# Kernel optimization log

Hardware: AMD Instinct MI355X
Metric: run time of the kernel (lower is better)

The kernel has to match this reference:

```python
import jax, jax.numpy as jnp
import numpy as np
from jax import lax

EOS_IDX = -1
N_POWERS = 7
B, L, D2 = 64, 81, 512      # batch, spatial_size, 2*inter_emb_size
S, C = 17, 256              # decode steps, candidates per step
V, H, E, P, F = 13042, 512, 80, 60, 178  # vocab, lstm_size, order_emb, power_emb, order-feat dim


def _lstm_cell(x, h, c, w_ih, w_hh, b_ih, b_hh):
    gates = x @ w_ih.T + b_ih + h @ w_hh.T + b_hh
    i, f, g, o = jnp.split(gates, 4, axis=-1)
    c_new = jax.nn.sigmoid(f) * c + jax.nn.sigmoid(i) * jnp.tanh(g)
    h_new = jax.nn.sigmoid(o) * jnp.tanh(c_new)
    return h_new, c_new


def _order_loc_feats(locs, enc_w, lin=None):
    # gather enc_w rows at candidate order locations; masked add == index_add_ with unique flat indices
    b = enc_w.shape[0]
    valid = locs > 0                                   # [B, C]
    safe = jnp.clip(locs, 0, enc_w.shape[1] - 1)
    g = enc_w[jnp.arange(b)[:, None], safe]            # [B, C, D]
    if lin is not None:
        g = g @ lin[0] + lin[1]
    return jnp.where(valid[..., None], g, jnp.zeros((), enc_w.dtype))


def setup_inputs() -> dict:
    key = jax.random.key(0)
    ks = jax.random.split(key, 40)
    w = lambda i, shape: jax.random.normal(ks[i], shape, dtype=jnp.float32) * 0.05
    return {
        'enc': jax.random.normal(ks[0], (B, L, D2), dtype=jnp.float32),
        'loc_idxs': jax.random.randint(ks[1], (B, L), 0, S),
        'all_cand_idxs': jax.random.randint(ks[2], (B, S, C), 0, V),
        'power': jax.random.randint(ks[3], (B, S), 0, N_POWERS),
        'teacher_force_orders': jax.random.randint(ks[4], (B, S), 0, V),
        'master_alignments': jax.random.uniform(ks[5], (L, L), dtype=jnp.float32),
        'order_embedding_w': w(6, (V, E)),
        'cand_embedding_w': w(7, (V, H)),
        'power_lin_w': w(8, (N_POWERS, P)),
        'power_lin_b': w(9, (P,)),
        'lstm_w_ih0': w(10, (4 * H, D2 + E + P)),
        'lstm_w_hh0': w(11, (4 * H, H)),
        'lstm_b_ih0': w(12, (4 * H,)),
        'lstm_b_hh0': w(13, (4 * H,)),
        'lstm_w_ih1': w(14, (4 * H, H)),
        'lstm_w_hh1': w(15, (4 * H, H)),
        'lstm_b_ih1': w(16, (4 * H,)),
        'lstm_b_hh1': w(17, (4 * H,)),
        'order_feats': jax.random.uniform(ks[18], (V, F), dtype=jnp.float32),
        'order_feat_lin_w': w(19, (F, E)),
        'order_feat_lin_b': w(20, (E,)),
        'order_decoder_w_w': w(21, (F, H)),
        'order_decoder_w_b': w(22, (H,)),
        'order_decoder_b_w': w(23, (F, 1)),
        'order_decoder_b_b': w(24, (1,)),
        'relfeat_src_w': w(25, (D2, H + 1)),
        'relfeat_src_b': w(26, (H + 1,)),
        'relfeat_dst_w': w(27, (D2, H + 1)),
        'relfeat_dst_b': w(28, (H + 1,)),
        'emb_relfeat_src_w': w(29, (E, H + 1)),
        'emb_relfeat_src_b': w(30, (H + 1,)),
        'emb_relfeat_dst_w': w(31, (E, H + 1)),
        'emb_relfeat_dst_b': w(32, (H + 1,)),
        'order_srcs': jax.random.randint(ks[33], (V,), -1, L),
        'order_dsts': jax.random.randint(ks[34], (V,), -1, L),
    }


def reference(enc, loc_idxs, all_cand_idxs, power, teacher_force_orders, master_alignments,
              order_embedding_w, cand_embedding_w, power_lin_w, power_lin_b,
              lstm_w_ih0, lstm_w_hh0, lstm_b_ih0, lstm_b_hh0,
              lstm_w_ih1, lstm_w_hh1, lstm_b_ih1, lstm_b_hh1,
              order_feats, order_feat_lin_w, order_feat_lin_b,
              order_decoder_w_w, order_decoder_w_b, order_decoder_b_w, order_decoder_b_b,
              relfeat_src_w, relfeat_src_b, relfeat_dst_w, relfeat_dst_b,
              emb_relfeat_src_w, emb_relfeat_src_b, emb_relfeat_dst_w, emb_relfeat_dst_b,
              order_srcs, order_dsts):
    b, l, d2 = enc.shape
    s = all_cand_idxs.shape[1]
    hsz = cand_embedding_w.shape[1]
    esz = order_embedding_w.shape[1]

    # compute_alignments for all steps at once: [S, B, L]
    steps = jnp.arange(s)
    mask = ((loc_idxs[None] == steps[:, None, None]) | (loc_idxs[None] == -2)).astype(enc.dtype)
    align = jnp.einsum('sbl,lm->sbm', mask, master_alignments)
    align = align / (align.sum(-1, keepdims=True) + 1e-5)
    loc_enc_all = jnp.einsum('sbl,bld->sbd', align, enc)            # [S, B, D2]

    power_1h = jax.nn.one_hot(jnp.clip(power, 0), N_POWERS, dtype=enc.dtype)
    power_embs = power_1h @ power_lin_w + power_lin_b               # [B, S, P]

    src_relfeat = enc @ relfeat_src_w + relfeat_src_b               # [B, L, H+1]
    dst_relfeat = enc @ relfeat_dst_w + relfeat_dst_b
    order_enc = jnp.zeros((b, l, esz), enc.dtype)                   # zeros per original init

    def body(carry, xs):
        h, c, order_emb = carry
        loc_enc, power_emb, cand_idxs, teacher = xs
        x = jnp.concatenate([loc_enc, order_emb, power_emb], axis=-1)
        h0, c0 = _lstm_cell(x, h[0], c[0], lstm_w_ih0, lstm_w_hh0, lstm_b_ih0, lstm_b_hh0)
        h1, c1 = _lstm_cell(h0, h[1], c[1], lstm_w_ih1, lstm_w_hh1, lstm_b_ih1, lstm_b_hh1)
        out = h1                                                    # [B, H]
        valid = cand_idxs != EOS_IDX
        safe_cand = jnp.clip(cand_idxs, 0)
        cand_emb = jnp.where(valid[..., None], cand_embedding_w[safe_cand], 0.0)
        logits = jnp.einsum('bch,bh->bc', cand_emb, out)
        feats = order_feats[safe_cand]                              # [B, C, F]
        order_w = jnp.concatenate([feats @ order_decoder_w_w + order_decoder_w_b,
                                   feats @ order_decoder_b_w + order_decoder_b_b], axis=-1)
        cand_srcs = order_srcs[safe_cand]
        cand_dsts = order_dsts[safe_cand]
        order_w = order_w + _order_loc_feats(cand_srcs, src_relfeat)
        order_w = order_w + _order_loc_feats(cand_dsts, dst_relfeat)
        order_w = order_w + _order_loc_feats(cand_srcs, order_enc, (emb_relfeat_src_w, emb_relfeat_src_b))
        order_w = order_w + _order_loc_feats(cand_dsts, order_enc, (emb_relfeat_dst_w, emb_relfeat_dst_b))
        out1 = jnp.concatenate([out, jnp.ones((out.shape[0], 1), out.dtype)], axis=-1)
        logits = logits + jnp.einsum('bcf,bf->bc', order_w, out1)
        logits = jnp.where(valid, logits, -1e9)
        local = jnp.argmax((cand_idxs == teacher[:, None]).astype(jnp.int32), axis=1)
        new_order_emb = order_embedding_w[teacher] + order_feats[teacher] @ order_feat_lin_w + order_feat_lin_b
        return (jnp.stack([h0, h1]), jnp.stack([c0, c1]), new_order_emb), (logits, local)

    init = (jnp.zeros((2, b, hsz), enc.dtype), jnp.zeros((2, b, hsz), enc.dtype), jnp.zeros((b, esz), enc.dtype))
    xs = (loc_enc_all, jnp.swapaxes(power_embs, 0, 1), jnp.swapaxes(all_cand_idxs, 0, 1), teacher_force_orders.T)
    _, (logits_all, local_all) = lax.scan(body, init, xs)
    logits = jnp.swapaxes(logits_all, 0, 1)                         # [B, S, C]
    local = jnp.swapaxes(local_all, 0, 1)
    return teacher_force_orders, local, logits


if __name__ == '__main__':
    outs = reference(**setup_inputs())
    print([o.shape for o in outs])
```

## Files before the change

kernel.cpp:

```cpp
#include <hip/hip_runtime.h>


#define NB 64
#define NL 81
#define ND2 512
#define NS 17
#define NC 256
#define NV 13042
#define NH 512
#define NE 80
#define NP 60
#define NF 178
#define NKX 652
#define NG4 2048
#define KSPLIT 8
#define NOUT (NB*NS*(2+NC))

#define OFF_XSTAT 0
#define OFF_PG    709376
#define OFF_PTMP  1757952
#define OFF_H0    2282240
#define OFF_C0    2315008
#define OFF_C1    2347776
#define OFF_X1    2380544
#define OFF_OUT   2446080
#define OFF_FP    2478912
#define OFF_SRC   2490432
#define WS_FLOATS 2500800

__device__ __forceinline__ float sigm(float x) { return 1.0f / (1.0f + expf(-x)); }

__global__ void k_out01(const int* cand, const int* teacher, float* out) {
    int i = blockIdx.x * 256 + threadIdx.x;
    if (i >= NB * NS) return;
    int tv = teacher[i];
    int mi = 0;
    const int* cr = cand + (long long)i * NC;
    for (int c = 0; c < NC; ++c) {
        if (cr[c] == tv) { mi = c; break; }
    }
    out[i] = (float)tv;
    out[NB * NS + i] = (float)mi;
}

__global__ void k_init(float* ws) {
    long long n = WS_FLOATS - OFF_H0;
    long long ob = (long long)OFF_OUT + 512 * 64 - OFF_H0;
    long long oe = ob + 64;
    for (long long i = (long long)blockIdx.x * 256 + threadIdx.x; i < n; i += (long long)gridDim.x * 256)
        ws[OFF_H0 + i] = (i >= ob && i < oe) ? 1.0f : 0.0f;
}

__global__ void k_locenc(const int* loc_idxs, const float* MA, const float* enc, float* xstat) {
    int s = blockIdx.x, b = blockIdx.y, t = threadIdx.x;
    __shared__ int loc[NL];
    __shared__ float al[NL];
    __shared__ float norm;
    if (t < NL) loc[t] = loc_idxs[b * NL + t];
    __syncthreads();
    if (t < NL) {
        float a = 0.0f;
        for (int l = 0; l < NL; ++l)
            if (loc[l] == s || loc[l] == -2) a += MA[l * NL + t];
        al[t] = a;
    }
    __syncthreads();
    if (t == 0) {
        float sm = 0.0f;
        for (int m = 0; m < NL; ++m) sm += al[m];
        norm = 1.0f / (sm + 1e-5f);
    }
    __syncthreads();
    float inv = norm;
    for (int d = t; d < ND2; d += 256) {
        float acc = 0.0f;
        for (int m = 0; m < NL; ++m) acc += al[m] * enc[((long long)b * NL + m) * ND2 + d];
        xstat[((long long)s * NKX + d) * 64 + b] = acc * inv;
    }
}

__global__ void k_embpow(const int* teacher, const int* power,
                         const float* oemb, const float* feats,
                         const float* oflw, const float* oflb,
                         const float* plw, const float* plb,
                         float* xstat) {
    int s = blockIdx.x, b = blockIdx.y, t = threadIdx.x;
    __shared__ float lf[NF];
    int tf = (s > 0) ? teacher[b * NS + (s - 1)] : 0;
    if (t < NF) lf[t] = feats[(long long)tf * NF + t];
    __syncthreads();
    if (t < NE) {
        float v = 0.0f;
        if (s > 0) {
            v = oemb[(long long)tf * NE + t] + oflb[t];
            for (int f = 0; f < NF; ++f) v += lf[f] * oflw[f * NE + t];
        }
        xstat[((long long)s * NKX + 512 + t) * 64 + b] = v;
    } else if (t < NE + NP) {
        int p = t - NE;
        int pw = power[b * NS + s];
        if (pw < 0) pw = 0;
        xstat[((long long)s * NKX + 592 + p) * 64 + b] = plw[pw * NP + p] + plb[p];
    }
}

__global__ void k_gemm(const float* xA, int KA, const float* xB, int KB,
                       const float* WA0, const float* WA1, const float* WB,
                       float* pout0, float* pout1,
                       int N, int kchunk) {
    const float* WA = blockIdx.y ? WA1 : WA0;
    float* pout = blockIdx.y ? pout1 : pout0;
    int wid = (blockIdx.x * 256 + threadIdx.x) >> 6;
    int lane = threadIdx.x & 63;
    int nps = N >> 3;
    int ks = wid / nps;
    if (ks >= KSPLIT) return;
    int n0 = (wid - ks * nps) << 3;
    int kbeg = ks * kchunk;
    int kend = KA + KB;
    if (kbeg + kchunk < kend) kend = kbeg + kchunk;
    float a0 = 0.f, a1 = 0.f, a2 = 0.f, a3 = 0.f, a4 = 0.f, a5 = 0.f, a6 = 0.f, a7 = 0.f;
    int kaend = (kend < KA) ? kend : KA;
    int k = kbeg;
    for (; k < kaend; ++k) {
        float xv = xA[k * 64 + lane];
        const float* w = WA + (long long)n0 * KA + k;
        a0 += xv * w[0 * (long long)KA]; a1 += xv * w[1 * (long long)KA];
        a2 += xv * w[2 * (long long)KA]; a3 += xv * w[3 * (long long)KA];
        a4 += xv * w[4 * (long long)KA]; a5 += xv * w[5 * (long long)KA];
        a6 += xv * w[6 * (long long)KA]; a7 += xv * w[7 * (long long)KA];
    }
    for (; k < kend; ++k) {
        int kk = k - KA;
        float xv = xB[kk * 64 + lane];
        const float* w = WB + (long long)n0 * KB + kk;
        a0 += xv * w[0 * (long long)KB]; a1 += xv * w[1 * (long long)KB];
        a2 += xv * w[2 * (long long)KB]; a3 += xv * w[3 * (long long)KB];
        a4 += xv * w[4 * (long long)KB]; a5 += xv * w[5 * (long long)KB];
        a6 += xv * w[6 * (long long)KB]; a7 += xv * w[7 * (long long)KB];
    }
    float* po = pout + ((long long)ks * N + n0) * 64 + lane;
    po[0] = a0; po[64] = a1; po[128] = a2; po[192] = a3;
    po[256] = a4; po[320] = a5; po[384] = a6; po[448] = a7;
}

__global__ void k_cell(const float* pg, const float* bih, const float* bhh,
                       float* cT, float* h1, float* h2) {
    int gid = blockIdx.x * 256 + threadIdx.x;
    int j = gid >> 6, b = gid & 63;
    float gi = bih[j] + bhh[j];
    float gf = bih[512 + j] + bhh[512 + j];
    float gg = bih[1024 + j] + bhh[1024 + j];
    float go = bih[1536 + j] + bhh[1536 + j];
    for (int ks = 0; ks < KSPLIT; ++ks) {
        const float* base = pg + (long long)ks * NG4 * 64;
        gi += base[j * 64 + b];
        gf += base[(512 + j) * 64 + b];
        gg += base[(1024 + j) * 64 + b];
        go += base[(1536 + j) * 64 + b];
    }
    float c = cT[j * 64 + b];
    float cn = sigm(gf) * c + sigm(gi) * tanhf(gg);
    float h = sigm(go) * tanhf(cn);
    cT[j * 64 + b] = cn;
    h1[j * 64 + b] = h;
    h2[j * 64 + b] = h;
}

__global__ void k_fproj(const float* outT, const float* odww, const float* odwb,
                        const float* odbw, const float* odbb, float* fp) {
    int b = blockIdx.x, t = threadIdx.x;
    __shared__ float oh[512];
    for (int d = t; d < 512; d += 256) oh[d] = outT[d * 64 + b];
    __syncthreads();
    if (t < NF) {
        float acc = odbw[t];
        const float* w = odww + (long long)t * 512;
        for (int h = 0; h < 512; ++h) acc += w[h] * oh[h];
        fp[b * 180 + t] = acc;
    } else if (t == NF) {
        float acc = odbb[0];
        for (int h = 0; h < 512; ++h) acc += odwb[h] * oh[h];
        fp[b * 180 + NF] = acc;
    }
}

__global__ void k_srcadd(const float* ptmp, const float* outT, const float* enc,
                         const float* rsb, const float* rdb,
                         const float* esb, const float* edb, float* srcadd) {
    int b = blockIdx.x, which = blockIdx.y, t = threadIdx.x;
    __shared__ float tmpc[512];
    __shared__ float red[256];
    const float* pt = ptmp + (long long)which * KSPLIT * 512 * 64;
    for (int d = t; d < 512; d += 256) {
        float v = 0.0f;
        for (int ks = 0; ks < KSPLIT; ++ks) v += pt[((long long)ks * 512 + d) * 64 + b];
        tmpc[d] = v;
    }
    const float* bb = which ? rdb : rsb;
    const float* be = which ? edb : esb;
    float p = 0.0f;
    for (int j = t; j < 513; j += 256) p += (bb[j] + be[j]) * outT[j * 64 + b];
    red[t] = p;
    __syncthreads();
    for (int off = 128; off > 0; off >>= 1) {
        if (t < off) red[t] += red[t + off];
        __syncthreads();
    }
    float sb = red[0];
    if (t < NL) {
        float acc = sb;
        const float* er = enc + ((long long)b * NL + t) * ND2;
        for (int d = 0; d < 512; ++d) acc += er[d] * tmpc[d];
        srcadd[((long long)which * 64 + b) * NL + t] = acc;
    }
}

__global__ void k_logits(const float* cemb, const float* feats, const float* outT,
                         const float* fp, const float* srcadd, const int* cand,
                         const int* osrc, const int* odst, int s, float* out) {
    int b = blockIdx.x, c = threadIdx.x;
    __shared__ float oh[512];
    __shared__ float sa[NL];
    __shared__ float da[NL];
    __shared__ float lfp[180];
    for (int d = c; d < 512; d += 256) oh[d] = outT[d * 64 + b];
    if (c < NL) {
        sa[c] = srcadd[(long long)b * NL + c];
        da[c] = srcadd[((long long)64 + b) * NL + c];
    }
    if (c < 180) lfp[c] = fp[b * 180 + c];
    __syncthreads();
    int cd = cand[((long long)b * NS + s) * NC + c];
    float res = -1e9f;
    if (cd >= 0) {
        float acc = lfp[NF];
        const float* row = cemb + (long long)cd * 512;
        for (int d = 0; d < 512; ++d) acc += row[d] * oh[d];
        const float* fr = feats + (long long)cd * NF;
        for (int f = 0; f < NF; ++f) acc += fr[f] * lfp[f];
        int sc = osrc[cd];
        if (sc > 0) acc += sa[sc];
        int dc = odst[cd];
        if (dc > 0) acc += da[dc];
        res = acc;
    }
    out[(long long)NB * NS * 2 + ((long long)b * NS + s) * NC + c] = res;
}

extern "C" void kernel_launch(void* const* d_in, const int* in_sizes, int n_in,
                              void* d_out, int out_size, void* d_ws, size_t ws_size,
                              hipStream_t stream) {
    float* out = (float*)d_out;

    const float* enc         = (const float*)d_in[0];
    const int*   loc_idxs    = (const int*)d_in[1];
    const int*   cand        = (const int*)d_in[2];
    const int*   power       = (const int*)d_in[3];
    const int*   teacher     = (const int*)d_in[4];
    const float* MA          = (const float*)d_in[5];
    const float* order_emb_w = (const float*)d_in[6];
    const float* cand_emb_w  = (const float*)d_in[7];
    const float* plw         = (const float*)d_in[8];
    const float* plb         = (const float*)d_in[9];
    const float* w_ih0       = (const float*)d_in[10];
    const float* w_hh0       = (const float*)d_in[11];
    const float* b_ih0       = (const float*)d_in[12];
    const float* b_hh0       = (const float*)d_in[13];
    const float* w_ih1       = (const float*)d_in[14];
    const float* w_hh1       = (const float*)d_in[15];
    const float* b_ih1       = (const float*)d_in[16];
    const float* b_hh1       = (const float*)d_in[17];
    const float* ofeats      = (const float*)d_in[18];
    const float* ofl_w       = (const float*)d_in[19];
    const float* ofl_b       = (const float*)d_in[20];
    const float* odw_w       = (const float*)d_in[21];
    const float* odw_b       = (const float*)d_in[22];
    const float* odb_w       = (const float*)d_in[23];
    const float* odb_b       = (const float*)d_in[24];
    const float* rsw         = (const float*)d_in[25];
    const float* rsb         = (const float*)d_in[26];
    const float* rdw         = (const float*)d_in[27];
    const float* rdb         = (const float*)d_in[28];
    const float* esb         = (const float*)d_in[30];
    const float* edb         = (const float*)d_in[32];
    const int*   osrc        = (const int*)d_in[33];
    const int*   odst        = (const int*)d_in[34];

    float* ws = (float*)d_ws;
    float* xstat  = ws + OFF_XSTAT;
    float* pg     = ws + OFF_PG;
    float* ptmp   = ws + OFF_PTMP;
    float* h0T    = ws + OFF_H0;
    float* c0T    = ws + OFF_C0;
    float* c1T    = ws + OFF_C1;
    float* x1T    = ws + OFF_X1;
    float* outT   = ws + OFF_OUT;
    float* fp     = ws + OFF_FP;
    float* srcadd = ws + OFF_SRC;

    k_out01<<<5, 256, 0, stream>>>(cand, teacher, out);
    k_init<<<256, 256, 0, stream>>>(ws);
    k_locenc<<<dim3(NS, NB), 256, 0, stream>>>(loc_idxs, MA, enc, xstat);
    k_embpow<<<dim3(NS, NB), 256, 0, stream>>>(teacher, power, order_emb_w, ofeats,
                                               ofl_w, ofl_b, plw, plb, xstat);
    for (int s = 0; s < NS; ++s) {
        k_gemm<<<dim3(512, 1), 256, 0, stream>>>(xstat + (long long)s * NKX * 64, NKX, h0T, 512,
                                                 w_ih0, (const float*)0, w_hh0,
                                                 pg, (float*)0, NG4, 146);
        k_cell<<<128, 256, 0, stream>>>(pg, b_ih0, b_hh0, c0T, x1T, h0T);
        k_gemm<<<dim3(512, 1), 256, 0, stream>>>(x1T, 512, x1T + (long long)512 * 64, 512,
                                                 w_ih1, (const float*)0, w_hh1,
                                                 pg, (float*)0, NG4, 128);
        k_cell<<<128, 256, 0, stream>>>(pg, b_ih1, b_hh1, c1T, outT, x1T + (long long)512 * 64);
        k_gemm<<<dim3(128, 2), 256, 0, stream>>>(outT, 513, (const float*)0, 0,
                                                 rsw, rdw, (const float*)0,
                                                 ptmp, ptmp + (long long)KSPLIT * 512 * 64, 512, 65);
        k_fproj<<<NB, 256, 0, stream>>>(outT, odw_w, odw_b, odb_w, odb_b, fp);
        k_srcadd<<<dim3(NB, 2), 256, 0, stream>>>(ptmp, outT, enc, rsb, rdb, esb, edb, srcadd);
        k_logits<<<NB, 256, 0, stream>>>(cand_emb_w, ofeats, outT, fp, srcadd, cand, osrc, odst, s, out);
    }
}
```

Baseline: 3.510 ms.

## Fuse LSTM gate GEMM with cell update and merge post-step projections into one kernel

```diff
diff --git a/kernel.cpp b/kernel.cpp
--- a/kernel.cpp
+++ b/kernel.cpp
@@ -12,21 +12,15 @@
 #define NP 60
 #define NF 178
 #define NKX 652
-#define NG4 2048
-#define KSPLIT 8
 #define NOUT (NB*NS*(2+NC))
 
 #define OFF_XSTAT 0
-#define OFF_PG    709376
-#define OFF_PTMP  1757952
-#define OFF_H0    2282240
-#define OFF_C0    2315008
-#define OFF_C1    2347776
-#define OFF_X1    2380544
-#define OFF_OUT   2446080
-#define OFF_FP    2478912
-#define OFF_SRC   2490432
-#define WS_FLOATS 2500800
+#define OFF_AL    709376
+#define OFF_H0    797504
+#define OFF_C0    863040
+#define OFF_C1    895808
+#define OFF_OT    928576
+#define WS_END    994240
 
 __device__ __forceinline__ float sigm(float x) { return 1.0f / (1.0f + expf(-x)); }
 
@@ -44,38 +38,61 @@
 }
 
 __global__ void k_init(float* ws) {
-    long long n = WS_FLOATS - OFF_H0;
-    long long ob = (long long)OFF_OUT + 512 * 64 - OFF_H0;
-    long long oe = ob + 64;
-    for (long long i = (long long)blockIdx.x * 256 + threadIdx.x; i < n; i += (long long)gridDim.x * 256)
-        ws[OFF_H0 + i] = (i >= ob && i < oe) ? 1.0f : 0.0f;
-}
-
-__global__ void k_locenc(const int* loc_idxs, const float* MA, const float* enc, float* xstat) {
-    int s = blockIdx.x, b = blockIdx.y, t = threadIdx.x;
+    long long n = WS_END - OFF_H0;
+    for (long long i = (long long)blockIdx.x * 256 + threadIdx.x; i < n;
+         i += (long long)gridDim.x * 256) {
+        long long a = OFF_H0 + i;
+        float v = 0.0f;
+        if (a >= OFF_OT) {
+            long long r = (a - OFF_OT) % 32832;
+            if ((r >> 6) == 512) v = 1.0f;
+        }
+        ws[a] = v;
+    }
+}
+
+__global__ void k_locenc2(const int* loc_idxs, const float* MA, const float* enc,
+                          float* xstat) {
+    int b = blockIdx.x, t = threadIdx.x;
+    __shared__ float sMA[NL * NL];
+    __shared__ float sAL[NS * NL];
+    __shared__ float sinv[NS];
     __shared__ int loc[NL];
-    __shared__ float al[NL];
-    __shared__ float norm;
     if (t < NL) loc[t] = loc_idxs[b * NL + t];
-    __syncthreads();
-    if (t < NL) {
+    for (int i = t; i < NL * NL; i += 256) sMA[i] = MA[i];
+    __syncthreads();
+    for (int idx = t; idx < NS * NL; idx += 256) {
+        int s = idx / NL, m = idx - s * NL;
         float a = 0.0f;
         for (int l = 0; l < NL; ++l)
-            if (loc[l] == s || loc[l] == -2) a += MA[l * NL + t];
-        al[t] = a;
-    }
-    __syncthreads();
-    if (t == 0) {
+            if (loc[l] == s || loc[l] == -2) a += sMA[l * NL + m];
+        sAL[idx] = a;
+    }
+    __syncthreads();
+    if (t < NS) {
         float sm = 0.0f;
-        for (int m = 0; m < NL; ++m) sm += al[m];
-        norm = 1.0f / (sm + 1e-5f);
-    }
-    __syncthreads();
-    float inv = norm;
-    for (int d = t; d < ND2; d += 256) {
-        float acc = 0.0f;
-        for (int m = 0; m < NL; ++m) acc += al[m] * enc[((long long)b * NL + m) * ND2 + d];
-        xstat[((long long)s * NKX + d) * 64 + b] = acc * inv;
+        for (int m = 0; m < NL; ++m) sm += sAL[t * NL + m];
+        sinv[t] = 1.0f / (sm + 1e-5f);
+    }
+    __syncthreads();
+    float acc0[NS], acc1[NS];
+#pragma unroll
+    for (int s = 0; s < NS; ++s) { acc0[s] = 0.0f; acc1[s] = 0.0f; }
+    const float* eb = enc + (long long)b * NL * ND2;
+    for (int m = 0; m < NL; ++m) {
+        float e0 = eb[m * ND2 + t];
+        float e1 = eb[m * ND2 + t + 256];
+#pragma unroll
+        for (int s = 0; s < NS; ++s) {
+            float a = sAL[s * NL + m];
+            acc0[s] += a * e0;
+            acc1[s] += a * e1;
+        }
+    }
+#pragma unroll
+    for (int s = 0; s < NS; ++s) {
+        xstat[((long long)s * NKX + t) * 64 + b] = acc0[s] * sinv[s];
+        xstat[((long long)s * NKX + t + 256) * 64 + b] = acc1[s] * sinv[s];
     }
 }
 
@@ -104,134 +121,110 @@
     }
 }
 
-__global__ void k_gemm(const float* xA, int KA, const float* xB, int KB,
-                       const float* WA0, const float* WA1, const float* WB,
-                       float* pout0, float* pout1,
-                       int N, int kchunk) {
-    const float* WA = blockIdx.y ? WA1 : WA0;
-    float* pout = blockIdx.y ? pout1 : pout0;
-    int wid = (blockIdx.x * 256 + threadIdx.x) >> 6;
-    int lane = threadIdx.x & 63;
-    int nps = N >> 3;
-    int ks = wid / nps;
-    if (ks >= KSPLIT) return;
-    int n0 = (wid - ks * nps) << 3;
-    int kbeg = ks * kchunk;
-    int kend = KA + KB;
-    if (kbeg + kchunk < kend) kend = kbeg + kchunk;
-    float a0 = 0.f, a1 = 0.f, a2 = 0.f, a3 = 0.f, a4 = 0.f, a5 = 0.f, a6 = 0.f, a7 = 0.f;
-    int kaend = (kend < KA) ? kend : KA;
-    int k = kbeg;
-    for (; k < kaend; ++k) {
-        float xv = xA[k * 64 + lane];
-        const float* w = WA + (long long)n0 * KA + k;
-        a0 += xv * w[0 * (long long)KA]; a1 += xv * w[1 * (long long)KA];
-        a2 += xv * w[2 * (long long)KA]; a3 += xv * w[3 * (long long)KA];
-        a4 += xv * w[4 * (long long)KA]; a5 += xv * w[5 * (long long)KA];
-        a6 += xv * w[6 * (long long)KA]; a7 += xv * w[7 * (long long)KA];
-    }
-    for (; k < kend; ++k) {
-        int kk = k - KA;
-        float xv = xB[kk * 64 + lane];
-        const float* w = WB + (long long)n0 * KB + kk;
-        a0 += xv * w[0 * (long long)KB]; a1 += xv * w[1 * (long long)KB];
-        a2 += xv * w[2 * (long long)KB]; a3 += xv * w[3 * (long long)KB];
-        a4 += xv * w[4 * (long long)KB]; a5 += xv * w[5 * (long long)KB];
-        a6 += xv * w[6 * (long long)KB]; a7 += xv * w[7 * (long long)KB];
-    }
-    float* po = pout + ((long long)ks * N + n0) * 64 + lane;
-    po[0] = a0; po[64] = a1; po[128] = a2; po[192] = a3;
-    po[256] = a4; po[320] = a5; po[384] = a6; po[448] = a7;
-}
-
-__global__ void k_cell(const float* pg, const float* bih, const float* bhh,
-                       float* cT, float* h1, float* h2) {
-    int gid = blockIdx.x * 256 + threadIdx.x;
-    int j = gid >> 6, b = gid & 63;
-    float gi = bih[j] + bhh[j];
-    float gf = bih[512 + j] + bhh[512 + j];
-    float gg = bih[1024 + j] + bhh[1024 + j];
-    float go = bih[1536 + j] + bhh[1536 + j];
-    for (int ks = 0; ks < KSPLIT; ++ks) {
-        const float* base = pg + (long long)ks * NG4 * 64;
-        gi += base[j * 64 + b];
-        gf += base[(512 + j) * 64 + b];
-        gg += base[(1024 + j) * 64 + b];
-        go += base[(1536 + j) * 64 + b];
-    }
-    float c = cT[j * 64 + b];
-    float cn = sigm(gf) * c + sigm(gi) * tanhf(gg);
-    float h = sigm(go) * tanhf(cn);
-    cT[j * 64 + b] = cn;
-    h1[j * 64 + b] = h;
-    h2[j * 64 + b] = h;
-}
-
-__global__ void k_fproj(const float* outT, const float* odww, const float* odwb,
-                        const float* odbw, const float* odbb, float* fp) {
+__global__ void k_lstm(const float* xA, int KA, const float* xB,
+                       const float* wA, const float* wB,
+                       const float* bih, const float* bhh,
+                       float* cT, float* hout) {
+    __shared__ float part[2][4][4][64];
+    int tid = threadIdx.x;
+    int b = tid & 63, jl = (tid >> 6) & 3, kh = tid >> 8;
+    int j = blockIdx.x * 4 + jl;
+    const float* x = kh ? xB : xA;
+    const float* w = kh ? wB : wA;
+    int K = kh ? 512 : KA;
+    const float4* w0 = (const float4*)(w + (long long)j * K);
+    const float4* w1 = (const float4*)(w + (long long)(512 + j) * K);
+    const float4* w2 = (const float4*)(w + (long long)(1024 + j) * K);
+    const float4* w3 = (const float4*)(w + (long long)(1536 + j) * K);
+    float a0 = 0.f, a1 = 0.f, a2 = 0.f, a3 = 0.f;
+    int K4 = K >> 2;
+    for (int k4 = 0; k4 < K4; ++k4) {
+        int k = k4 << 2;
+        float x0 = x[(k + 0) * 64 + b];
+        float x1 = x[(k + 1) * 64 + b];
+        float x2 = x[(k + 2) * 64 + b];
+        float x3 = x[(k + 3) * 64 + b];
+        float4 q0 = w0[k4], q1 = w1[k4], q2 = w2[k4], q3 = w3[k4];
+        a0 += q0.x * x0 + q0.y * x1 + q0.z * x2 + q0.w * x3;
+        a1 += q1.x * x0 + q1.y * x1 + q1.z * x2 + q1.w * x3;
+        a2 += q2.x * x0 + q2.y * x1 + q2.z * x2 + q2.w * x3;
+        a3 += q3.x * x0 + q3.y * x1 + q3.z * x2 + q3.w * x3;
+    }
+    part[kh][jl][0][b] = a0;
+    part[kh][jl][1][b] = a1;
+    part[kh][jl][2][b] = a2;
+    part[kh][jl][3][b] = a3;
+    __syncthreads();
+    if (kh == 0) {
+        float gi = a0 + part[1][jl][0][b] + bih[j] + bhh[j];
+        float gf = a1 + part[1][jl][1][b] + bih[512 + j] + bhh[512 + j];
+        float gg = a2 + part[1][jl][2][b] + bih[1024 + j] + bhh[1024 + j];
+        float go = a3 + part[1][jl][3][b] + bih[1536 + j] + bhh[1536 + j];
+        float c = cT[j * 64 + b];
+        float cn = sigm(gf) * c + sigm(gi) * tanhf(gg);
+        float h = sigm(go) * tanhf(cn);
+        cT[j * 64 + b] = cn;
+        hout[j * 64 + b] = h;
+    }
+}
+
+__global__ void k_post(const float* otcur, const float* enc,
+                       const float* rsw, const float* rsb,
+                       const float* rdw, const float* rdb,
+                       const float* esb, const float* edb,
+                       const float* odww, const float* odwb,
+                       const float* odbw, const float* odbb,
+                       const float* cemb, const float* feats,
+                       const int* cand, const int* osrc, const int* odst,
+                       int s, float* out) {
     int b = blockIdx.x, t = threadIdx.x;
-    __shared__ float oh[512];
-    for (int d = t; d < 512; d += 256) oh[d] = outT[d * 64 + b];
-    __syncthreads();
+    __shared__ float oh[513];
+    __shared__ float tmpc[2][512];
+    __shared__ float lfp[180];
+    __shared__ float sb[2];
+    __shared__ float sa[NL];
+    __shared__ float da[NL];
+    for (int d = t; d < 513; d += 256) oh[d] = otcur[d * 64 + b];
+    __syncthreads();
+#pragma unroll
+    for (int r = 0; r < 4; ++r) {
+        int idx = t + 256 * r;
+        int which = idx >> 9, d = idx & 511;
+        const float* w = (which ? rdw : rsw) + (long long)d * 513;
+        float acc = 0.0f;
+        for (int c = 0; c < 513; ++c) acc += w[c] * oh[c];
+        tmpc[which][d] = acc;
+    }
     if (t < NF) {
+        const float* w = odww + (long long)t * 512;
         float acc = odbw[t];
-        const float* w = odww + (long long)t * 512;
         for (int h = 0; h < 512; ++h) acc += w[h] * oh[h];
-        fp[b * 180 + t] = acc;
+        lfp[t] = acc;
     } else if (t == NF) {
         float acc = odbb[0];
         for (int h = 0; h < 512; ++h) acc += odwb[h] * oh[h];
-        fp[b * 180 + NF] = acc;
-    }
-}
-
-__global__ void k_srcadd(const float* ptmp, const float* outT, const float* enc,
-                         const float* rsb, const float* rdb,
-                         const float* esb, const float* edb, float* srcadd) {
-    int b = blockIdx.x, which = blockIdx.y, t = threadIdx.x;
-    __shared__ float tmpc[512];
-    __shared__ float red[256];
-    const float* pt = ptmp + (long long)which * KSPLIT * 512 * 64;
-    for (int d = t; d < 512; d += 256) {
-        float v = 0.0f;
-        for (int ks = 0; ks < KSPLIT; ++ks) v += pt[((long long)ks * 512 + d) * 64 + b];
-        tmpc[d] = v;
-    }
-    const float* bb = which ? rdb : rsb;
-    const float* be = which ? edb : esb;
-    float p = 0.0f;
-    for (int j = t; j < 513; j += 256) p += (bb[j] + be[j]) * outT[j * 64 + b];
-    red[t] = p;
-    __syncthreads();
-    for (int off = 128; off > 0; off >>= 1) {
-        if (t < off) red[t] += red[t + off];
-        __syncthreads();
-    }
-    float sb = red[0];
-    if (t < NL) {
-        float acc = sb;
-        const float* er = enc + ((long long)b * NL + t) * ND2;
-        for (int d = 0; d < 512; ++d) acc += er[d] * tmpc[d];
-        srcadd[((long long)which * 64 + b) * NL + t] = acc;
-    }
-}
-
-__global__ void k_logits(const float* cemb, const float* feats, const float* outT,
-                         const float* fp, const float* srcadd, const int* cand,
-                         const int* osrc, const int* odst, int s, float* out) {
-    int b = blockIdx.x, c = threadIdx.x;
-    __shared__ float oh[512];
-    __shared__ float sa[NL];
-    __shared__ float da[NL];
-    __shared__ float lfp[180];
-    for (int d = c; d < 512; d += 256) oh[d] = outT[d * 64 + b];
-    if (c < NL) {
-        sa[c] = srcadd[(long long)b * NL + c];
-        da[c] = srcadd[((long long)64 + b) * NL + c];
-    }
-    if (c < 180) lfp[c] = fp[b * 180 + c];
-    __syncthreads();
-    int cd = cand[((long long)b * NS + s) * NC + c];
+        lfp[NF] = acc;
+    } else if (t == 179) {
+        float acc = 0.0f;
+        for (int c = 0; c < 513; ++c) acc += (rsb[c] + esb[c]) * oh[c];
+        sb[0] = acc;
+    } else if (t == 180) {
+        float acc = 0.0f;
+        for (int c = 0; c < 513; ++c) acc += (rdb[c] + edb[c]) * oh[c];
+        sb[1] = acc;
+    }
+    __syncthreads();
+    if (t < 2 * NL) {
+        int which = (t >= NL) ? 1 : 0;
+        int l = which ? (t - NL) : t;
+        const float* er = enc + ((long long)b * NL + l) * ND2;
+        const float* tc = tmpc[which];
+        float acc = sb[which];
+        for (int d = 0; d < 512; ++d) acc += er[d] * tc[d];
+        if (which) da[l] = acc; else sa[l] = acc;
+    }
+    __syncthreads();
+    int cd = cand[((long long)b * NS + s) * NC + t];
     float res = -1e9f;
     if (cd >= 0) {
         float acc = lfp[NF];
@@ -245,7 +238,7 @@
         if (dc > 0) acc += da[dc];
         res = acc;
     }
-    out[(long long)NB * NS * 2 + ((long long)b * NS + s) * NC + c] = res;
+    out[(long long)NB * NS * 2 + ((long long)b * NS + s) * NC + t] = res;
 }
 
 extern "C" void kernel_launch(void* const* d_in, const int* in_sizes, int n_in,
@@ -288,36 +281,29 @@
     const int*   odst        = (const int*)d_in[34];
 
     float* ws = (float*)d_ws;
-    float* xstat  = ws + OFF_XSTAT;
-    float* pg     = ws + OFF_PG;
-    float* ptmp   = ws + OFF_PTMP;
-    float* h0T    = ws + OFF_H0;
-    float* c0T    = ws + OFF_C0;
-    float* c1T    = ws + OFF_C1;
-    float* x1T    = ws + OFF_X1;
-    float* outT   = ws + OFF_OUT;
-    float* fp     = ws + OFF_FP;
-    float* srcadd = ws + OFF_SRC;
+    float* xstat = ws + OFF_XSTAT;
+    float* H0    = ws + OFF_H0;
+    float* c0T   = ws + OFF_C0;
+    float* c1T   = ws + OFF_C1;
+    float* OT    = ws + OFF_OT;
 
     k_out01<<<5, 256, 0, stream>>>(cand, teacher, out);
-    k_init<<<256, 256, 0, stream>>>(ws);
-    k_locenc<<<dim3(NS, NB), 256, 0, stream>>>(loc_idxs, MA, enc, xstat);
+    k_init<<<64, 256, 0, stream>>>(ws);
+    k_locenc2<<<NB, 256, 0, stream>>>(loc_idxs, MA, enc, xstat);
     k_embpow<<<dim3(NS, NB), 256, 0, stream>>>(teacher, power, order_emb_w, ofeats,
                                                ofl_w, ofl_b, plw, plb, xstat);
+
     for (int s = 0; s < NS; ++s) {
-        k_gemm<<<dim3(512, 1), 256, 0, stream>>>(xstat + (long long)s * NKX * 64, NKX, h0T, 512,
-                                                 w_ih0, (const float*)0, w_hh0,
-                                                 pg, (float*)0, NG4, 146);
-        k_cell<<<128, 256, 0, stream>>>(pg, b_ih0, b_hh0, c0T, x1T, h0T);
-        k_gemm<<<dim3(512, 1), 256, 0, stream>>>(x1T, 512, x1T + (long long)512 * 64, 512,
-                                                 w_ih1, (const float*)0, w_hh1,
-                                                 pg, (float*)0, NG4, 128);
-        k_cell<<<128, 256, 0, stream>>>(pg, b_ih1, b_hh1, c1T, outT, x1T + (long long)512 * 64);
-        k_gemm<<<dim3(128, 2), 256, 0, stream>>>(outT, 513, (const float*)0, 0,
-                                                 rsw, rdw, (const float*)0,
-                                                 ptmp, ptmp + (long long)KSPLIT * 512 * 64, 512, 65);
-        k_fproj<<<NB, 256, 0, stream>>>(outT, odw_w, odw_b, odb_w, odb_b, fp);
-        k_srcadd<<<dim3(NB, 2), 256, 0, stream>>>(ptmp, outT, enc, rsb, rdb, esb, edb, srcadd);
-        k_logits<<<NB, 256, 0, stream>>>(cand_emb_w, ofeats, outT, fp, srcadd, cand, osrc, odst, s, out);
-    }
-}
+        float* h0in   = H0 + (s & 1) * 32768;
+        float* h0out  = H0 + ((s + 1) & 1) * 32768;
+        float* otprev = OT + (s & 1) * 32832;
+        float* otcur  = OT + ((s + 1) & 1) * 32832;
+        k_lstm<<<128, 512, 0, stream>>>(xstat + (long long)s * NKX * 64, NKX, h0in,
+                                        w_ih0, w_hh0, b_ih0, b_hh0, c0T, h0out);
+        k_lstm<<<128, 512, 0, stream>>>(h0out, 512, otprev,
+                                        w_ih1, w_hh1, b_ih1, b_hh1, c1T, otcur);
+        k_post<<<NB, 256, 0, stream>>>(otcur, enc, rsw, rsb, rdw, rdb, esb, edb,
+                                       odw_w, odw_b, odb_w, odb_b,
+                                       cand_emb_w, ofeats, cand, osrc, odst, s, out);
+    }
+}
```

Measured after the change: 4.660 ms. 32.8% more time.
